# Optimization experiments

Measured on AMD Instinct MI355X. Metric: run time of the kernel, lower is better.

The kernel has to match this reference:

```python
import jax, jax.numpy as jnp
import numpy as np

B, N, D, W = 4, 4096, 256, 7
K = 2 * W + 1  # 15 taps: positions [i-2w, ..., i]
H = 4 * D
EPS = 1e-5


def layer_norm(x, g, b):
    mu = jnp.mean(x, axis=-1, keepdims=True)
    var = jnp.mean(jnp.square(x - mu), axis=-1, keepdims=True)
    return (x - mu) * jax.lax.rsqrt(var + EPS) * g + b


def setup_inputs() -> dict:
    key = jax.random.key(0)
    ks = jax.random.split(key, 8)
    s = 0.02
    return {
        "x": jax.random.normal(ks[0], (B, N, D), dtype=jnp.float32),
        # w_mix[k] is the DxD block of the (K*D -> D) Linear acting on offset k-2w
        "w_mix": (jax.random.normal(ks[1], (K, D, D), dtype=jnp.float32) * s),
        "b_mix": jnp.zeros((D,), dtype=jnp.float32),
        "g1": jnp.ones((D,), jnp.float32) + 0.1 * jax.random.normal(ks[2], (D,), jnp.float32),
        "b1": 0.1 * jax.random.normal(ks[3], (D,), jnp.float32),
        "w_ff1": jax.random.normal(ks[4], (D, H), dtype=jnp.float32) * s,
        "b_ff1": jnp.zeros((H,), dtype=jnp.float32),
        "w_ff2": jax.random.normal(ks[5], (H, D), dtype=jnp.float32) * s,
        "b_ff2": jnp.zeros((D,), dtype=jnp.float32),
        "g2": jnp.ones((D,), jnp.float32) + 0.1 * jax.random.normal(ks[6], (D,), jnp.float32),
        "b2": 0.1 * jax.random.normal(ks[7], (D,), jnp.float32),
    }


def reference(x, w_mix, b_mix, g1, b1, w_ff1, b_ff1, w_ff2, b_ff2, g2, b2):
    # Causal windowed concat + Linear == causal 1D conv with kernel K=2w+1.
    # torch feats chunk k holds x[i - 2w + k]; conv tap k with left pad 2w
    # sees exactly x[i - 2w + k], so kernel = mix weight reshaped (K, D, D).
    mix = jax.lax.conv_general_dilated(
        x, w_mix, window_strides=(1,), padding=[(2 * W, 0)],
        dimension_numbers=("NWC", "WIO", "NWC"),
    ) + b_mix  # [B, N, D]
    # Dropout is identity in eval mode (reference baseline).
    h = layer_norm(x + mix, g1, b1)
    ff = jnp.dot(jax.nn.gelu(jnp.dot(h, w_ff1) + b_ff1, approximate=False), w_ff2) + b_ff2
    return layer_norm(h + ff, g2, b2)
```

## Files before the change

kernel.cpp:

```cpp
#include <hip/hip_runtime.h>
#include <cstdint>

#define DD     256
#define HH     1024
#define NNSEQ  4096
#define MT     64
#define XR     78
#define XPITCH 264
#define SLOTP  260
#define EPSLN  1e-5f

typedef unsigned short u16;
typedef __attribute__((ext_vector_type(8))) short short8;
typedef __attribute__((ext_vector_type(4))) float f32x4;

#define MFMA(a, b, c) __builtin_amdgcn_mfma_f32_16x16x32_bf16(a, b, c, 0, 0, 0)

__device__ __forceinline__ u16 f2bf(float f) {
  unsigned u = __float_as_uint(f);
  u += 0x7FFF + ((u >> 16) & 1);
  return (u16)(u >> 16);
}
__device__ __forceinline__ float bf2f(u16 s) { return __uint_as_float(((unsigned)s) << 16); }

__device__ __forceinline__ float fast_gelu(float v) {
  const float e = __expf(v * __builtin_fmaf(v * v, -0.0713548163f, -1.5957691216f));
  return v * __builtin_amdgcn_rcpf(1.f + e);
}

__global__ __launch_bounds__(256) void k_prep(
    const float* __restrict__ wmix, const float* __restrict__ wff1,
    const float* __restrict__ wff2, u16* __restrict__ wpk,
    u16* __restrict__ w1pk, u16* __restrict__ w2pk)
{
  __shared__ float t[32][257];
  const int b = blockIdx.x, tid = threadIdx.x;

  u16* dst;
  if (b < 120) {
    dst = wpk + (size_t)b * 8192;
    for (int r = 0; r < 32; ++r)
      t[r][tid] = wmix[(size_t)(b * 32 + r) * 256 + tid];
  } else if (b < 152) {
    const int u = b - 120, c2 = u >> 3, s = u & 7;
    dst = w1pk + (size_t)u * 8192;
    for (int r = 0; r < 32; ++r)
      t[r][tid] = wff1[(size_t)(s * 32 + r) * 1024 + c2 * 256 + tid];
  } else {
    const int u = b - 152, c2 = u >> 3, s = u & 7;
    dst = w2pk + (size_t)u * 8192;
    for (int r = 0; r < 32; ++r)
      t[r][tid] = wff2[(size_t)(c2 * 256 + s * 32 + r) * 256 + tid];
  }
  __syncthreads();

  const int l = tid & 63, q = l >> 4, cl = l & 15;
#pragma unroll
  for (int f = 0; f < 4; ++f) {
    const int fi = f * 4 + (tid >> 6);
    const int n = fi * 16 + cl;
    uint4 pk;
    unsigned* p = (unsigned*)&pk;
#pragma unroll
    for (int jj = 0; jj < 4; ++jj)
      p[jj] = (unsigned)f2bf(t[q * 8 + jj * 2][n]) | ((unsigned)f2bf(t[q * 8 + jj * 2 + 1][n]) << 16);
    *(uint4*)&dst[(size_t)fi * 512 + l * 8] = pk;
  }
}

__global__ __launch_bounds__(1024, 4) void k_fused(
    const float* __restrict__ x, const u16* __restrict__ wpk,
    const float* __restrict__ bmix, const float* __restrict__ g1,
    const float* __restrict__ b1, const u16* __restrict__ w1pk,
    const float* __restrict__ bf1, const u16* __restrict__ w2pk,
    const float* __restrict__ bf2, const float* __restrict__ g2,
    const float* __restrict__ b2, float* __restrict__ out)
{
  __shared__ __align__(16) u16 bufA[XR * XPITCH];
  __shared__ __align__(16) u16 asbuf[2 * MT * XPITCH];
  __shared__ float redS[8][MT], redS2[8][MT];
  __shared__ float muL[MT], invL[MT];

#define bufB ((float*)asbuf)

  const int tid = threadIdx.x;
  const int wv = tid >> 6, l = tid & 63, q = l >> 4, cl = l & 15;
  const int rg = wv >> 3;
  const int mgq = (wv >> 2) & 1;
  const int ng = wv & 3;
  const int cg = wv & 7;
  const long tok0 = (long)blockIdx.x * MT;
  const int n0 = (int)(tok0 & (NNSEQ - 1));

  f32x4 acc[2][4];
#pragma unroll
  for (int nt = 0; nt < 4; ++nt) {
    const float bm = (mgq == 0) ? bmix[ng * 64 + nt * 16 + cl] : 0.f;
#pragma unroll
    for (int mt = 0; mt < 2; ++mt) acc[mt][nt] = (f32x4){bm, bm, bm, bm};
  }
  const u16* bbase = wpk + (size_t)(mgq * 60) * 8192 + (size_t)(ng * 4) * 512 + (size_t)l * 8;

  {
    const int cslot = l * 4;
    for (int r = wv; r < XR; r += 16) {
      const int nloc = n0 - 14 + r;
      float4 v = make_float4(0.f, 0.f, 0.f, 0.f);
      if (nloc >= 0) v = *(const float4*)&x[(tok0 - 14 + r) * DD + cslot];
      uint2 pk;
      pk.x = (unsigned)f2bf(v.x) | ((unsigned)f2bf(v.y) << 16);
      pk.y = (unsigned)f2bf(v.z) | ((unsigned)f2bf(v.w) << 16);
      *(uint2*)&bufA[r * XPITCH + cslot] = pk;
    }
  }

#define LOAD_A(dst, s_)                                                         \
  {                                                                             \
    const int ks = mgq * 60 + (s_);                                             \
    const int xrow = ks >> 3, c0 = (ks & 7) * 32;                               \
    _Pragma("unroll")                                                           \
    for (int mt = 0; mt < 2; ++mt)                                              \
      dst[mt] = *(const short8*)&bufA[(xrow + rg * 32 + mt * 16 + cl) * XPITCH + c0 + q * 8]; \
  }
#define LOAD_B(dst, s_)                                                         \
  {                                                                             \
    const u16* bp = bbase + (size_t)(s_) * 8192;                                \
    _Pragma("unroll")                                                           \
    for (int nt = 0; nt < 4; ++nt)                                              \
      dst[nt] = *(const short8*)(bp + nt * 512);                                \
  }

  {
    short8 af[3][2], bfr[3][4];
    LOAD_B(bfr[0], 0)
    LOAD_B(bfr[1], 1)
    LOAD_B(bfr[2], 2)
    __syncthreads();
    LOAD_A(af[0], 0)
    LOAD_A(af[1], 1)
    LOAD_A(af[2], 2)

    for (int sb = 0; sb < 57; sb += 3) {
#pragma unroll
      for (int u = 0; u < 3; ++u) {
#pragma unroll
        for (int mt = 0; mt < 2; ++mt)
#pragma unroll
          for (int nt = 0; nt < 4; ++nt)
            acc[mt][nt] = MFMA(af[u][mt], bfr[u][nt], acc[mt][nt]);
        LOAD_A(af[u], sb + u + 3)
        LOAD_B(bfr[u], sb + u + 3)
      }
    }
#pragma unroll
    for (int u = 0; u < 3; ++u) {
#pragma unroll
      for (int mt = 0; mt < 2; ++mt)
#pragma unroll
        for (int nt = 0; nt < 4; ++nt)
          acc[mt][nt] = MFMA(af[u][mt], bfr[u][nt], acc[mt][nt]);
    }
  }
#undef LOAD_A
#undef LOAD_B

  if (mgq == 1) {
#pragma unroll
    for (int mt = 0; mt < 2; ++mt)
#pragma unroll
      for (int nt = 0; nt < 4; ++nt)
#pragma unroll
        for (int reg = 0; reg < 4; ++reg)
          bufB[(rg * 32 + mt * 16 + q * 4 + reg) * SLOTP + ng * 64 + nt * 16 + cl] = acc[mt][nt][reg];
  }
  __syncthreads();

  if (mgq == 0) {
    float ps[2][4], ps2[2][4];
#pragma unroll
    for (int mt = 0; mt < 2; ++mt)
#pragma unroll
      for (int reg = 0; reg < 4; ++reg) {
        const int row = rg * 32 + mt * 16 + q * 4 + reg;
        float s = 0.f, s2 = 0.f;
#pragma unroll
        for (int nt = 0; nt < 4; ++nt) {
          const int col = ng * 64 + nt * 16 + cl;
          const float y = acc[mt][nt][reg] + bufB[row * SLOTP + col]
                        + x[(tok0 + row) * DD + col];
          acc[mt][nt][reg] = y;
          s += y; s2 += y * y;
        }
#pragma unroll
        for (int off = 1; off < 16; off <<= 1) { s += __shfl_xor(s, off, 64); s2 += __shfl_xor(s2, off, 64); }
        ps[mt][reg] = s; ps2[mt][reg] = s2;
      }
    if (cl == 0) {
#pragma unroll
      for (int mt = 0; mt < 2; ++mt)
#pragma unroll
        for (int reg = 0; reg < 4; ++reg) {
          const int row = rg * 32 + mt * 16 + q * 4 + reg;
          redS[ng][row] = ps[mt][reg]; redS2[ng][row] = ps2[mt][reg];
        }
    }
  }
  __syncthreads();
  if (tid < MT) {
    const float s  = redS[0][tid] + redS[1][tid] + redS[2][tid] + redS[3][tid];
    const float s2 = redS2[0][tid] + redS2[1][tid] + redS2[2][tid] + redS2[3][tid];
    const float mu = s * (1.f / DD);
    const float var = s2 * (1.f / DD) - mu * mu;
    muL[tid] = mu; invL[tid] = rsqrtf(var + EPSLN);
  }
  __syncthreads();

  if (mgq == 0) {
#pragma unroll
    for (int nt = 0; nt < 4; ++nt) {
      const int col = ng * 64 + nt * 16 + cl;
      const float gv = g1[col], bv = b1[col];
#pragma unroll
      for (int mt = 0; mt < 2; ++mt)
#pragma unroll
        for (int reg = 0; reg < 4; ++reg) {
          const int row = rg * 32 + mt * 16 + q * 4 + reg;
          const float hv = (acc[mt][nt][reg] - muL[row]) * invL[row] * gv + bv;
          bufA[row * XPITCH + col] = f2bf(hv);
        }
    }
  }
  __syncthreads();

  f32x4 acc2[2][2];
#pragma unroll
  for (int nt = 0; nt < 2; ++nt) {
    const float bv = bf2[cg * 32 + nt * 16 + cl];
#pragma unroll
    for (int mt = 0; mt < 2; ++mt) acc2[mt][nt] = (f32x4){bv, bv, bv, bv};
  }

#define FF_LDA(src, dst, s_)                                                    \
  {                                                                             \
    _Pragma("unroll")                                                           \
    for (int mt = 0; mt < 2; ++mt)                                              \
      dst[mt] = *(const short8*)&src[(rg * 32 + mt * 16 + cl) * XPITCH + (s_) * 32 + q * 8]; \
  }
#define FF_LDB(wsrc, dst, s_)                                                   \
  {                                                                             \
    const u16* bp = wsrc + (size_t)(c * 8 + (s_)) * 8192 + (size_t)(cg * 2) * 512 + (size_t)l * 8; \
    _Pragma("unroll")                                                           \
    for (int nt = 0; nt < 2; ++nt)                                              \
      dst[nt] = *(const short8*)(bp + nt * 512);                                \
  }

  for (int c = 0; c < 4; ++c) {
    u16* asb = asbuf + (c & 1) * (MT * XPITCH);
    f32x4 acc1[2][2];
#pragma unroll
    for (int nt = 0; nt < 2; ++nt) {
      const float bv = bf1[c * 256 + cg * 32 + nt * 16 + cl];
#pragma unroll
      for (int mt = 0; mt < 2; ++mt) acc1[mt][nt] = (f32x4){bv, bv, bv, bv};
    }
    {
      short8 a2[2][2], b2r[2][2];
      FF_LDA(bufA, a2[0], 0) FF_LDB(w1pk, b2r[0], 0)
      FF_LDA(bufA, a2[1], 1) FF_LDB(w1pk, b2r[1], 1)
#pragma unroll
      for (int s = 0; s < 6; ++s) {
        const int cur = s & 1;
#pragma unroll
        for (int mt = 0; mt < 2; ++mt)
#pragma unroll
          for (int nt = 0; nt < 2; ++nt)
            acc1[mt][nt] = MFMA(a2[cur][mt], b2r[cur][nt], acc1[mt][nt]);
        FF_LDA(bufA, a2[cur], s + 2) FF_LDB(w1pk, b2r[cur], s + 2)
      }
#pragma unroll
      for (int s = 6; s < 8; ++s) {
        const int cur = s & 1;
#pragma unroll
        for (int mt = 0; mt < 2; ++mt)
#pragma unroll
          for (int nt = 0; nt < 2; ++nt)
            acc1[mt][nt] = MFMA(a2[cur][mt], b2r[cur][nt], acc1[mt][nt]);
      }
    }
#pragma unroll
    for (int mt = 0; mt < 2; ++mt)
#pragma unroll
      for (int nt = 0; nt < 2; ++nt)
#pragma unroll
        for (int reg = 0; reg < 4; ++reg) {
          const float g = fast_gelu(acc1[mt][nt][reg]);
          asb[(rg * 32 + mt * 16 + q * 4 + reg) * XPITCH + cg * 32 + nt * 16 + cl] = f2bf(g);
        }
    __syncthreads();
    {
      short8 a2[2][2], b2r[2][2];
      FF_LDA(asb, a2[0], 0) FF_LDB(w2pk, b2r[0], 0)
      FF_LDA(asb, a2[1], 1) FF_LDB(w2pk, b2r[1], 1)
#pragma unroll
      for (int s = 0; s < 6; ++s) {
        const int cur = s & 1;
#pragma unroll
        for (int mt = 0; mt < 2; ++mt)
#pragma unroll
          for (int nt = 0; nt < 2; ++nt)
            acc2[mt][nt] = MFMA(a2[cur][mt], b2r[cur][nt], acc2[mt][nt]);
        FF_LDA(asb, a2[cur], s + 2) FF_LDB(w2pk, b2r[cur], s + 2)
      }
#pragma unroll
      for (int s = 6; s < 8; ++s) {
        const int cur = s & 1;
#pragma unroll
        for (int mt = 0; mt < 2; ++mt)
#pragma unroll
          for (int nt = 0; nt < 2; ++nt)
            acc2[mt][nt] = MFMA(a2[cur][mt], b2r[cur][nt], acc2[mt][nt]);
      }
    }
  }
#undef FF_LDA
#undef FF_LDB

  {
    float ps[2][4], ps2[2][4];
#pragma unroll
    for (int mt = 0; mt < 2; ++mt)
#pragma unroll
      for (int reg = 0; reg < 4; ++reg) {
        const int row = rg * 32 + mt * 16 + q * 4 + reg;
        float s = 0.f, s2 = 0.f;
#pragma unroll
        for (int nt = 0; nt < 2; ++nt) {
          const int col = cg * 32 + nt * 16 + cl;
          const float y = acc2[mt][nt][reg] + bf2f(bufA[row * XPITCH + col]);
          acc2[mt][nt][reg] = y;
          s += y; s2 += y * y;
        }
#pragma unroll
        for (int off = 1; off < 16; off <<= 1) { s += __shfl_xor(s, off, 64); s2 += __shfl_xor(s2, off, 64); }
        ps[mt][reg] = s; ps2[mt][reg] = s2;
      }
    if (cl == 0) {
#pragma unroll
      for (int mt = 0; mt < 2; ++mt)
#pragma unroll
        for (int reg = 0; reg < 4; ++reg) {
          const int row = rg * 32 + mt * 16 + q * 4 + reg;
          redS[cg][row] = ps[mt][reg]; redS2[cg][row] = ps2[mt][reg];
        }
    }
  }
  __syncthreads();
  if (tid < MT) {
    float s = 0.f, s2 = 0.f;
#pragma unroll
    for (int k = 0; k < 8; ++k) { s += redS[k][tid]; s2 += redS2[k][tid]; }
    const float mu = s * (1.f / DD);
    const float var = s2 * (1.f / DD) - mu * mu;
    muL[tid] = mu; invL[tid] = rsqrtf(var + EPSLN);
  }
  __syncthreads();

#pragma unroll
  for (int nt = 0; nt < 2; ++nt) {
    const int col = cg * 32 + nt * 16 + cl;
    const float gv = g2[col], bv = b2[col];
#pragma unroll
    for (int mt = 0; mt < 2; ++mt)
#pragma unroll
      for (int reg = 0; reg < 4; ++reg) {
        const int row = rg * 32 + mt * 16 + q * 4 + reg;
        out[(tok0 + row) * DD + col] = (acc2[mt][nt][reg] - muL[row]) * invL[row] * gv + bv;
      }
  }
#undef bufB
}

extern "C" void kernel_launch(void* const* d_in, const int* in_sizes, int n_in,
                              void* d_out, int out_size, void* d_ws, size_t ws_size,
                              hipStream_t stream) {
  const float* x    = (const float*)d_in[0];
  const float* wmix = (const float*)d_in[1];
  const float* bmix = (const float*)d_in[2];
  const float* g1   = (const float*)d_in[3];
  const float* b1   = (const float*)d_in[4];
  const float* wff1 = (const float*)d_in[5];
  const float* bff1 = (const float*)d_in[6];
  const float* wff2 = (const float*)d_in[7];
  const float* bff2 = (const float*)d_in[8];
  const float* g2   = (const float*)d_in[9];
  const float* b2   = (const float*)d_in[10];
  float* out = (float*)d_out;

  u16* wpk  = (u16*)d_ws;
  u16* w1pk = wpk + 983040;
  u16* w2pk = w1pk + 262144;

  k_prep<<<184, 256, 0, stream>>>(wmix, wff1, wff2, wpk, w1pk, w2pk);

  k_fused<<<256, 1024, 0, stream>>>(x, wpk, bmix, g1, b1,
                                    w1pk, bff1, w2pk, bff2, g2, b2, out);
}
```

Baseline: 157.4 us.

## Retile conv-mix GEMM so each wave covers all rows and 32 columns

Changes the wave-to-tile mapping in the windowed-conv GEMM. Previously there were 2 row groups, 2 K halves and 4 column groups of 64. Now there are 2 K halves and 8 column groups of 32, and each wave covers all 64 rows. Each wave loads more A fragments from LDS and fewer weight fragments from global memory, and the software pipeline drops from 3-deep to 2-deep prefetch. The aim is to cut redundant global weight traffic per block, at the cost of more LDS reads and less latency hiding.

Result: faster. 149.8 us (-4.9%).

```diff
diff --git a/kernel.cpp b/kernel.cpp
--- a/kernel.cpp
+++ b/kernel.cpp
@@ -85,21 +85,21 @@
 
   const int tid = threadIdx.x;
   const int wv = tid >> 6, l = tid & 63, q = l >> 4, cl = l & 15;
+  const int mgq = wv >> 3;
+  const int ng = wv & 7;
   const int rg = wv >> 3;
-  const int mgq = (wv >> 2) & 1;
-  const int ng = wv & 3;
   const int cg = wv & 7;
   const long tok0 = (long)blockIdx.x * MT;
   const int n0 = (int)(tok0 & (NNSEQ - 1));
 
-  f32x4 acc[2][4];
-#pragma unroll
-  for (int nt = 0; nt < 4; ++nt) {
-    const float bm = (mgq == 0) ? bmix[ng * 64 + nt * 16 + cl] : 0.f;
-#pragma unroll
-    for (int mt = 0; mt < 2; ++mt) acc[mt][nt] = (f32x4){bm, bm, bm, bm};
-  }
-  const u16* bbase = wpk + (size_t)(mgq * 60) * 8192 + (size_t)(ng * 4) * 512 + (size_t)l * 8;
+  f32x4 acc[4][2];
+#pragma unroll
+  for (int nt = 0; nt < 2; ++nt) {
+    const float bm = (mgq == 0) ? bmix[ng * 32 + nt * 16 + cl] : 0.f;
+#pragma unroll
+    for (int mt = 0; mt < 4; ++mt) acc[mt][nt] = (f32x4){bm, bm, bm, bm};
+  }
+  const u16* bbase = wpk + (size_t)(mgq * 60) * 8192 + (size_t)(ng * 2) * 512 + (size_t)l * 8;
 
   {
     const int cslot = l * 4;
@@ -119,46 +119,37 @@
     const int ks = mgq * 60 + (s_);                                             \
     const int xrow = ks >> 3, c0 = (ks & 7) * 32;                               \
     _Pragma("unroll")                                                           \
-    for (int mt = 0; mt < 2; ++mt)                                              \
-      dst[mt] = *(const short8*)&bufA[(xrow + rg * 32 + mt * 16 + cl) * XPITCH + c0 + q * 8]; \
+    for (int mt = 0; mt < 4; ++mt)                                              \
+      dst[mt] = *(const short8*)&bufA[(xrow + mt * 16 + cl) * XPITCH + c0 + q * 8]; \
   }
 #define LOAD_B(dst, s_)                                                         \
   {                                                                             \
     const u16* bp = bbase + (size_t)(s_) * 8192;                                \
     _Pragma("unroll")                                                           \
-    for (int nt = 0; nt < 4; ++nt)                                              \
+    for (int nt = 0; nt < 2; ++nt)                                              \
       dst[nt] = *(const short8*)(bp + nt * 512);                                \
   }
 
   {
-    short8 af[3][2], bfr[3][4];
+    short8 af[2][4], bfr[2][2];
     LOAD_B(bfr[0], 0)
     LOAD_B(bfr[1], 1)
-    LOAD_B(bfr[2], 2)
     __syncthreads();
     LOAD_A(af[0], 0)
     LOAD_A(af[1], 1)
-    LOAD_A(af[2], 2)
-
-    for (int sb = 0; sb < 57; sb += 3) {
-#pragma unroll
-      for (int u = 0; u < 3; ++u) {
-#pragma unroll
-        for (int mt = 0; mt < 2; ++mt)
-#pragma unroll
-          for (int nt = 0; nt < 4; ++nt)
-            acc[mt][nt] = MFMA(af[u][mt], bfr[u][nt], acc[mt][nt]);
-        LOAD_A(af[u], sb + u + 3)
-        LOAD_B(bfr[u], sb + u + 3)
-      }
-    }
-#pragma unroll
-    for (int u = 0; u < 3; ++u) {
-#pragma unroll
-      for (int mt = 0; mt < 2; ++mt)
-#pragma unroll
-        for (int nt = 0; nt < 4; ++nt)
-          acc[mt][nt] = MFMA(af[u][mt], bfr[u][nt], acc[mt][nt]);
+
+#pragma unroll 2
+    for (int s = 0; s < 60; ++s) {
+      const int cur = s & 1;
+#pragma unroll
+      for (int mt = 0; mt < 4; ++mt)
+#pragma unroll
+        for (int nt = 0; nt < 2; ++nt)
+          acc[mt][nt] = MFMA(af[cur][mt], bfr[cur][nt], acc[mt][nt]);
+      if (s + 2 < 60) {
+        LOAD_A(af[cur], s + 2)
+        LOAD_B(bfr[cur], s + 2)
+      }
     }
   }
 #undef LOAD_A
@@ -166,26 +157,26 @@
 
   if (mgq == 1) {
 #pragma unroll
-    for (int mt = 0; mt < 2; ++mt)
-#pragma unroll
-      for (int nt = 0; nt < 4; ++nt)
+    for (int mt = 0; mt < 4; ++mt)
+#pragma unroll
+      for (int nt = 0; nt < 2; ++nt)
 #pragma unroll
         for (int reg = 0; reg < 4; ++reg)
-          bufB[(rg * 32 + mt * 16 + q * 4 + reg) * SLOTP + ng * 64 + nt * 16 + cl] = acc[mt][nt][reg];
+          bufB[(mt * 16 + q * 4 + reg) * SLOTP + ng * 32 + nt * 16 + cl] = acc[mt][nt][reg];
   }
   __syncthreads();
 
   if (mgq == 0) {
-    float ps[2][4], ps2[2][4];
-#pragma unroll
-    for (int mt = 0; mt < 2; ++mt)
+    float ps[4][4], ps2[4][4];
+#pragma unroll
+    for (int mt = 0; mt < 4; ++mt)
 #pragma unroll
       for (int reg = 0; reg < 4; ++reg) {
-        const int row = rg * 32 + mt * 16 + q * 4 + reg;
+        const int row = mt * 16 + q * 4 + reg;
         float s = 0.f, s2 = 0.f;
 #pragma unroll
-        for (int nt = 0; nt < 4; ++nt) {
-          const int col = ng * 64 + nt * 16 + cl;
+        for (int nt = 0; nt < 2; ++nt) {
+          const int col = ng * 32 + nt * 16 + cl;
           const float y = acc[mt][nt][reg] + bufB[row * SLOTP + col]
                         + x[(tok0 + row) * DD + col];
           acc[mt][nt][reg] = y;
@@ -197,18 +188,19 @@
       }
     if (cl == 0) {
 #pragma unroll
-      for (int mt = 0; mt < 2; ++mt)
+      for (int mt = 0; mt < 4; ++mt)
 #pragma unroll
         for (int reg = 0; reg < 4; ++reg) {
-          const int row = rg * 32 + mt * 16 + q * 4 + reg;
+          const int row = mt * 16 + q * 4 + reg;
           redS[ng][row] = ps[mt][reg]; redS2[ng][row] = ps2[mt][reg];
         }
     }
   }
   __syncthreads();
   if (tid < MT) {
-    const float s  = redS[0][tid] + redS[1][tid] + redS[2][tid] + redS[3][tid];
-    const float s2 = redS2[0][tid] + redS2[1][tid] + redS2[2][tid] + redS2[3][tid];
+    float s = 0.f, s2 = 0.f;
+#pragma unroll
+    for (int k = 0; k < 8; ++k) { s += redS[k][tid]; s2 += redS2[k][tid]; }
     const float mu = s * (1.f / DD);
     const float var = s2 * (1.f / DD) - mu * mu;
     muL[tid] = mu; invL[tid] = rsqrtf(var + EPSLN);
@@ -217,14 +209,14 @@
 
   if (mgq == 0) {
 #pragma unroll
-    for (int nt = 0; nt < 4; ++nt) {
-      const int col = ng * 64 + nt * 16 + cl;
+    for (int nt = 0; nt < 2; ++nt) {
+      const int col = ng * 32 + nt * 16 + cl;
       const float gv = g1[col], bv = b1[col];
 #pragma unroll
-      for (int mt = 0; mt < 2; ++mt)
+      for (int mt = 0; mt < 4; ++mt)
 #pragma unroll
         for (int reg = 0; reg < 4; ++reg) {
-          const int row = rg * 32 + mt * 16 + q * 4 + reg;
+          const int row = mt * 16 + q * 4 + reg;
           const float hv = (acc[mt][nt][reg] - muL[row]) * invL[row] * gv + bv;
           bufA[row * XPITCH + col] = f2bf(hv);
         }
```
